# Performance work log

Hardware: AMD Instinct MI355X
Metric: run time of the kernel (lower is better)

The kernel has to match this reference:

```python
import jax, jax.numpy as jnp
import numpy as np

HEADS = 8
EPS = 1e-6
LN_EPS = 1e-5


def avg_pool(x, k):
    b, c, h, w = x.shape
    return x.reshape(b, c, h // k, k, w // k, k).mean(axis=(3, 5))


def layernorm(x, g, b):
    mu = x.mean(-1, keepdims=True)
    var = x.var(-1, keepdims=True)
    return (x - mu) / jnp.sqrt(var + LN_EPS) * g + b


def pos_embed_2d(h, w, c):
    # original calls build_2d_sincos_position_embedding(w=h, h=w): grid over (h, w), row-major flatten
    gw, gh = jnp.meshgrid(jnp.arange(h, dtype=jnp.float32),
                          jnp.arange(w, dtype=jnp.float32), indexing='ij')
    pd = c // 4
    omega = 1.0 / (10000.0 ** (jnp.arange(pd, dtype=jnp.float32) / pd))
    ow = gw.reshape(-1, 1) * omega  # (h*w, pd)
    oh = gh.reshape(-1, 1) * omega
    return jnp.concatenate([jnp.sin(ow), jnp.cos(ow), jnp.sin(oh), jnp.cos(oh)], axis=1)  # (h*w, c)


def _forward(a3, a4, q_w, q_b, q_ln_g, q_ln_b, k_w, k_b, k_ln_g, k_ln_b,
             v_w, v_b, out_w, out_b, lin1_w, lin1_b, lin2_w, lin2_b,
             n1_g, n1_b, n2_g, n2_b, idx):
    orig_a3 = a3
    if idx == 2:
        a3d = avg_pool(a3, 2)
    else:
        a3d = avg_pool(a3, 4)
        a4 = avg_pool(a4, 2)
    bs, c, h, w = a3d.shape
    L = h * w  # tgt_len == src_len (a3_down and a4 have equal spatial size)
    hd = c // HEADS

    residual = a3d.reshape(bs, c, L).transpose(0, 2, 1)  # (b, L, c)
    x3 = residual
    x4 = a4.reshape(bs, c, L).transpose(0, 2, 1)
    pos = pos_embed_2d(h, w, c)  # (L, c)
    x3 = x3 + pos[None]
    x4 = x4 + pos[None]

    Q = layernorm(x3 @ q_w + q_b, q_ln_g, q_ln_b)
    K = layernorm(x4 @ k_w + k_b, k_ln_g, k_ln_b)
    V = x4 @ v_w + v_b
    Q = jax.nn.relu(Q).reshape(bs, L, HEADS, hd).transpose(0, 2, 1, 3)  # (b,h,L,d)
    K = jax.nn.relu(K).reshape(bs, L, HEADS, hd).transpose(0, 2, 1, 3)
    V = V.reshape(bs, L, HEADS, hd).transpose(0, 2, 1, 3)

    # cosFormer position reweighting: index = pi/2 * (1..m) / m
    m = L
    wi = (np.pi / 2.0) * jnp.arange(1, m + 1, dtype=jnp.float32) / m  # (m,)
    sn = jnp.sin(wi)[None, None, :, None]
    cs = jnp.cos(wi)[None, None, :, None]
    Q_ = jnp.concatenate([Q * sn, Q * cs], axis=-1)  # (b,h,L,2d)
    K_ = jnp.concatenate([K * sn, K * cs], axis=-1)

    KV = jnp.einsum('bhld,bhlm->bhdm', K_, V)                     # (b,h,2d,d)
    Z = 1.0 / jnp.maximum(jnp.einsum('bhld,bhd->bhl', Q_, K_.sum(axis=2)), EPS)
    attn = jnp.einsum('bhld,bhdm->bhlm', Q_, KV) * Z[..., None]   # (b,h,L,d)
    attn = attn.transpose(0, 2, 1, 3).reshape(bs, L, c)

    out = attn @ out_w + out_b
    out = layernorm(out, n1_g, n1_b)     # normalize_before=False -> norm1 applied
    out = residual + out                 # dropout=0
    res2 = out
    out = jax.nn.gelu(out @ lin1_w + lin1_b, approximate=False) @ lin2_w + lin2_b
    out = layernorm(out, n2_g, n2_b)
    out = res2 + out

    a3sa = out.transpose(0, 2, 1).reshape(bs, c, h, w)
    a3sa = jax.image.resize(a3sa, orig_a3.shape, method='bilinear')  # align_corners=False
    return a3sa * orig_a3


def setup_inputs() -> dict:
    key = jax.random.key(0)
    ks = jax.random.split(key, 10)
    B, C = 16, 256
    C4 = 4 * C

    def w(k, shp):
        return jax.random.normal(k, shp, dtype=jnp.float32) * 0.02

    return {
        'a3': jax.random.normal(ks[0], (B, C, 128, 128), dtype=jnp.float32),
        'a4': jax.random.normal(ks[1], (B, C, 64, 64), dtype=jnp.float32),
        'q_w': w(ks[2], (C, C)), 'q_b': jnp.zeros((C,), jnp.float32),
        'q_ln_g': jnp.ones((C,), jnp.float32), 'q_ln_b': jnp.zeros((C,), jnp.float32),
        'k_w': w(ks[3], (C, C)), 'k_b': jnp.zeros((C,), jnp.float32),
        'k_ln_g': jnp.ones((C,), jnp.float32), 'k_ln_b': jnp.zeros((C,), jnp.float32),
        'v_w': w(ks[4], (C, C)), 'v_b': jnp.zeros((C,), jnp.float32),
        'out_w': w(ks[5], (C, C)), 'out_b': jnp.zeros((C,), jnp.float32),
        'lin1_w': w(ks[6], (C, C4)), 'lin1_b': jnp.zeros((C4,), jnp.float32),
        'lin2_w': w(ks[7], (C4, C)), 'lin2_b': jnp.zeros((C,), jnp.float32),
        'n1_g': jnp.ones((C,), jnp.float32), 'n1_b': jnp.zeros((C,), jnp.float32),
        'n2_g': jnp.ones((C,), jnp.float32), 'n2_b': jnp.zeros((C,), jnp.float32),
        'idx': 2,
    }


def reference(a3, a4, q_w, q_b, q_ln_g, q_ln_b, k_w, k_b, k_ln_g, k_ln_b,
              v_w, v_b, out_w, out_b, lin1_w, lin1_b, lin2_w, lin2_b,
              n1_g, n1_b, n2_g, n2_b, idx):
    return _forward(a3, a4, q_w, q_b, q_ln_g, q_ln_b, k_w, k_b, k_ln_g, k_ln_b,
                    v_w, v_b, out_w, out_b, lin1_w, lin1_b, lin2_w, lin2_b,
                    n1_g, n1_b, n2_g, n2_b, idx)
```

## Files before the change

kernel.cpp:

```cpp
#include <hip/hip_runtime.h>
#include <hip/hip_bf16.h>
#include <math.h>

#define HEADS 8
#define LL 4096
#define CDIM 256
#define BATCH 16
#define NROWS (BATCH*LL)

typedef __attribute__((ext_vector_type(8))) __bf16 bf16x8;
typedef __attribute__((ext_vector_type(4))) float f32x4;

__device__ inline float b2f(ushort u) {
    union { unsigned u; float f; } v; v.u = ((unsigned)u) << 16; return v.f;
}
__device__ inline ushort f2b(float f) {
    union { float f; unsigned u; } v; v.f = f;
    unsigned r = (v.u + 0x7FFF + ((v.u >> 16) & 1)) >> 16;
    return (ushort)r;
}
__device__ inline void gload16(const void* g, void* l) {
    __builtin_amdgcn_global_load_lds(
        (const __attribute__((address_space(1))) unsigned int*)g,
        (__attribute__((address_space(3))) unsigned int*)l, 16, 0, 0);
}
template<int N> __device__ inline void wait_vmcnt() {
    asm volatile("s_waitcnt vmcnt(%0)" :: "n"(N) : "memory");
}
__device__ inline float fast_gelu(float v) {
    float u = 0.7978845608028654f * v * (1.0f + 0.044715f * v * v);
    float e = exp2f(u * 2.885390081777927f);
    float t = 1.0f - 2.0f / (e + 1.0f);
    return 0.5f * v * (1.0f + t);
}

__global__ __launch_bounds__(256) void prep_kernel(
    float* __restrict__ pos, float* __restrict__ snc,
    const float* __restrict__ q_w, const float* __restrict__ k_w,
    const float* __restrict__ v_w, const float* __restrict__ o_w,
    const float* __restrict__ w1, const float* __restrict__ w2,
    ushort* __restrict__ wqT, ushort* __restrict__ wkT,
    ushort* __restrict__ wvT, ushort* __restrict__ woT,
    ushort* __restrict__ w1T, ushort* __restrict__ w2T,
    float* __restrict__ ksglob)
{
    __shared__ float t[32][33];
    int bid = blockIdx.x;
    int tid = threadIdx.x;
    if (bid == 1792) {
        for (int i = tid; i < BATCH * 2 * 256; i += 256) ksglob[i] = 0.0f;
        return;
    }
    if (bid < 1024) {
        int c = tid;
        int k = c & 63;
        float omega = expf(-(float)k * (9.210340371976184f / 64.0f));
        #pragma unroll
        for (int i = 0; i < 4; ++i) {
            int l = bid * 4 + i;
            int y = l >> 6, x = l & 63;
            float coord = (c < 128) ? (float)y : (float)x;
            float ang = coord * omega;
            float val = ((c & 127) < 64) ? sinf(ang) : cosf(ang);
            pos[l * CDIM + c] = val;
            if (c < 2) {
                float wi = 1.5707963267948966f * (float)(l + 1) / (float)LL;
                snc[l * 2 + c] = (c == 0) ? sinf(wi) : cosf(wi);
            }
        }
        return;
    }
    int id = bid - 1024;
    const float* W; ushort* Wt; int K, N, kb, nb;
    if (id < 64)       { W = q_w; Wt = wqT; K = 256;  N = 256;  kb = (id & 7) * 32;  nb = (id >> 3) * 32; }
    else if (id < 128) { id -= 64;  W = k_w; Wt = wkT; K = 256;  N = 256;  kb = (id & 7) * 32;  nb = (id >> 3) * 32; }
    else if (id < 192) { id -= 128; W = v_w; Wt = wvT; K = 256;  N = 256;  kb = (id & 7) * 32;  nb = (id >> 3) * 32; }
    else if (id < 256) { id -= 192; W = o_w; Wt = woT; K = 256;  N = 256;  kb = (id & 7) * 32;  nb = (id >> 3) * 32; }
    else if (id < 512) { id -= 256; W = w1;  Wt = w1T; K = 256;  N = 1024; kb = (id & 7) * 32;  nb = (id >> 3) * 32; }
    else               { id -= 512; W = w2;  Wt = w2T; K = 1024; N = 256;  kb = (id & 31) * 32; nb = (id >> 5) * 32; }
    int x = tid & 31, y = tid >> 5;
    #pragma unroll
    for (int i = 0; i < 4; ++i)
        t[y + i * 8][x] = W[(size_t)(kb + y + i * 8) * N + nb + x];
    __syncthreads();
    #pragma unroll
    for (int i = 0; i < 4; ++i) {
        int n = y + i * 8;
        Wt[(size_t)(nb + n) * K + kb + x] = f2b(t[x][n]);
    }
}

__global__ __launch_bounds__(256) void pool_x3_kernel(
    const float* __restrict__ a3, ushort* __restrict__ residual,
    ushort* __restrict__ x3b, const float* __restrict__ pos)
{
    __shared__ float raw[64][128];
    __shared__ float pooled[64][65];
    int i = blockIdx.x, ct = blockIdx.y, b = blockIdx.z;
    int tid = threadIdx.x;
    #pragma unroll
    for (int it = 0; it < 8; ++it) {
        int lin = (it * 256 + tid) * 4;
        int x = lin & 127;
        int cc = lin >> 7;
        size_t base = ((size_t)(b * 256 + ct * 64 + cc) * 128 + 2 * i) * 128 + x;
        float4 v0 = *(const float4*)&a3[base];
        float4 v1 = *(const float4*)&a3[base + 128];
        float4 s = make_float4(v0.x + v1.x, v0.y + v1.y, v0.z + v1.z, v0.w + v1.w);
        *(float4*)&raw[cc][x] = s;
    }
    __syncthreads();
    #pragma unroll
    for (int it = 0; it < 16; ++it) {
        int idx = it * 256 + tid;
        int j = idx & 63, cc = idx >> 6;
        pooled[cc][j] = 0.25f * (raw[cc][2 * j] + raw[cc][2 * j + 1]);
    }
    __syncthreads();
    #pragma unroll
    for (int it = 0; it < 16; ++it) {
        int cc = tid & 63;
        int jj = (tid >> 6) + it * 4;
        float val = pooled[cc][jj];
        int l = i * 64 + jj;
        int c = ct * 64 + cc;
        size_t o = (size_t)(b * LL + l) * CDIM + c;
        residual[o] = f2b(val);
        x3b[o] = f2b(val + pos[l * CDIM + c]);
    }
}

__global__ __launch_bounds__(256) void x4_kernel(
    const float* __restrict__ a4, ushort* __restrict__ x4b, const float* __restrict__ pos)
{
    __shared__ float t2[64][65];
    int y = blockIdx.x, ct = blockIdx.y, b = blockIdx.z, tid = threadIdx.x;
    #pragma unroll
    for (int it = 0; it < 16; ++it) {
        int idx = it * 256 + tid;
        int x = idx & 63, cc = idx >> 6;
        t2[cc][x] = a4[((size_t)(b * 256 + ct * 64 + cc) * 64 + y) * 64 + x];
    }
    __syncthreads();
    #pragma unroll
    for (int it = 0; it < 16; ++it) {
        int cc = tid & 63;
        int xx = (tid >> 6) + it * 4;
        int l = y * 64 + xx, c = ct * 64 + cc;
        x4b[(size_t)(b * LL + l) * CDIM + c] = f2b(t2[cc][xx] + pos[l * CDIM + c]);
    }
}

template<int KSTEPS, bool DO_LN, bool DO_RELU, bool DO_GELU, bool DO_RES, bool DO_KSUM>
__global__ __launch_bounds__(512, 2) void gemm_mfma(
    const ushort* __restrict__ A, const ushort* __restrict__ Wt,
    const float* __restrict__ bias, const float* __restrict__ gam_,
    const float* __restrict__ bet_, const ushort* __restrict__ res,
    const float* __restrict__ snc, float* __restrict__ ksglob,
    ushort* __restrict__ outb, int colsTot)
{
    constexpr int K = KSTEPS * 32;
    __shared__ ushort As[3][128 * 32];
    __shared__ ushort Bs[3][256 * 32];
    __shared__ float redS[128][4];
    __shared__ float redQ[128][4];
    __shared__ float2 mustd[128];

    const int tid = threadIdx.x;
    const int lane = tid & 63;
    const int wv = tid >> 6;
    const int wr = wv >> 2;
    const int wc = wv & 3;
    const int wvu = __builtin_amdgcn_readfirstlane(wv);
    const int row0 = blockIdx.x * 128;
    const int cbBase = blockIdx.y * 256;

    const int sr = tid >> 2;
    const int sg = (tid & 3) ^ ((sr >> 1) & 3);
    const ushort* aSrc = A + (size_t)(row0 + sr) * K + sg * 8;
    const ushort* bSrc0 = Wt + (size_t)(cbBase + sr) * K + sg * 8;
    const ushort* bSrc1 = Wt + (size_t)(cbBase + 128 + sr) * K + sg * 8;

    const int frSlot = (lane >> 4) ^ (((lane & 15) >> 1) & 3);

    auto issue = [&](int t, int buf) {
        gload16(aSrc + t * 32, (char*)&As[buf][0] + wvu * 1024);
        gload16(bSrc0 + t * 32, (char*)&Bs[buf][0] + wvu * 1024);
        gload16(bSrc1 + t * 32, (char*)&Bs[buf][0] + 8192 + wvu * 1024);
    };

    f32x4 acc[4][4] = {};
    issue(0, 0); issue(1, 1);
    #pragma unroll
    for (int t = 0; t < KSTEPS; ++t) {
        if (t < KSTEPS - 1) wait_vmcnt<3>(); else wait_vmcnt<0>();
        __builtin_amdgcn_s_barrier();
        if (t + 2 < KSTEPS) issue(t + 2, (t + 2) % 3);
        const int cb = t % 3;
        bf16x8 af[4], bfr[4];
        #pragma unroll
        for (int f = 0; f < 4; ++f) {
            int r = wr * 64 + f * 16 + (lane & 15);
            af[f] = *(const bf16x8*)&As[cb][r * 32 + frSlot * 8];
            int c = wc * 64 + f * 16 + (lane & 15);
            bfr[f] = *(const bf16x8*)&Bs[cb][c * 32 + frSlot * 8];
        }
        #pragma unroll
        for (int fi = 0; fi < 4; ++fi)
            #pragma unroll
            for (int fj = 0; fj < 4; ++fj)
                acc[fi][fj] = __builtin_amdgcn_mfma_f32_16x16x32_bf16(
                    af[fi], bfr[fj], acc[fi][fj], 0, 0, 0);
    }
    __syncthreads();

    const int cl = lane & 15;
    const int rg = lane >> 4;
    float bia[4], gmv[4], btv[4];
    #pragma unroll
    for (int fj = 0; fj < 4; ++fj) {
        int col = cbBase + wc * 64 + fj * 16 + cl;
        bia[fj] = bias[col];
        if constexpr (DO_LN) { gmv[fj] = gam_[col]; btv[fj] = bet_[col]; }
    }
    #pragma unroll
    for (int fi = 0; fi < 4; ++fi)
        #pragma unroll
        for (int fj = 0; fj < 4; ++fj)
            #pragma unroll
            for (int j = 0; j < 4; ++j)
                acc[fi][fj][j] += bia[fj];

    if constexpr (DO_LN) {
        #pragma unroll
        for (int fi = 0; fi < 4; ++fi)
            #pragma unroll
            for (int j = 0; j < 4; ++j) {
                float s = acc[fi][0][j] + acc[fi][1][j] + acc[fi][2][j] + acc[fi][3][j];
                float q = acc[fi][0][j] * acc[fi][0][j] + acc[fi][1][j] * acc[fi][1][j]
                        + acc[fi][2][j] * acc[fi][2][j] + acc[fi][3][j] * acc[fi][3][j];
                #pragma unroll
                for (int m = 1; m <= 8; m <<= 1) {
                    s += __shfl_xor(s, m, 64);
                    q += __shfl_xor(q, m, 64);
                }
                if (cl == 0) {
                    int tr = wr * 64 + fi * 16 + rg * 4 + j;
                    redS[tr][wc] = s; redQ[tr][wc] = q;
                }
            }
        __syncthreads();
        if (tid < 128) {
            float s = redS[tid][0] + redS[tid][1] + redS[tid][2] + redS[tid][3];
            float q = redQ[tid][0] + redQ[tid][1] + redQ[tid][2] + redQ[tid][3];
            float mu = s * (1.0f / 256.0f);
            float var = q * (1.0f / 256.0f) - mu * mu;
            mustd[tid] = make_float2(mu, rsqrtf(var + 1e-5f));
        }
        __syncthreads();
        #pragma unroll
        for (int fi = 0; fi < 4; ++fi)
            #pragma unroll
            for (int j = 0; j < 4; ++j) {
                float2 ms = mustd[wr * 64 + fi * 16 + rg * 4 + j];
                #pragma unroll
                for (int fj = 0; fj < 4; ++fj)
                    acc[fi][fj][j] = (acc[fi][fj][j] - ms.x) * ms.y * gmv[fj] + btv[fj];
            }
    }
    if constexpr (DO_RELU) {
        #pragma unroll
        for (int fi = 0; fi < 4; ++fi)
            #pragma unroll
            for (int fj = 0; fj < 4; ++fj)
                #pragma unroll
                for (int j = 0; j < 4; ++j)
                    acc[fi][fj][j] = fmaxf(acc[fi][fj][j], 0.0f);
    }
    if constexpr (DO_GELU) {
        #pragma unroll
        for (int fi = 0; fi < 4; ++fi)
            #pragma unroll
            for (int fj = 0; fj < 4; ++fj)
                #pragma unroll
                for (int j = 0; j < 4; ++j)
                    acc[fi][fj][j] = fast_gelu(acc[fi][fj][j]);
    }
    float kss[4] = {}, ksc[4] = {};
    #pragma unroll
    for (int fi = 0; fi < 4; ++fi)
        #pragma unroll
        for (int j = 0; j < 4; ++j) {
            int rloc = wr * 64 + fi * 16 + rg * 4 + j;
            size_t row = row0 + rloc;
            size_t rbase = row * (size_t)colsTot + cbBase + wc * 64 + cl;
            float sn, cs;
            if constexpr (DO_KSUM) {
                int l = (int)(row & (LL - 1));
                sn = snc[l * 2]; cs = snc[l * 2 + 1];
            }
            #pragma unroll
            for (int fj = 0; fj < 4; ++fj) {
                float v = acc[fi][fj][j];
                if constexpr (DO_RES) v += b2f(res[rbase + fj * 16]);
                outb[rbase + fj * 16] = f2b(v);
                if constexpr (DO_KSUM) { kss[fj] += sn * v; ksc[fj] += cs * v; }
            }
        }
    if constexpr (DO_KSUM) {
        int b = row0 >> 12;
        #pragma unroll
        for (int fj = 0; fj < 4; ++fj) {
            float s = kss[fj], c = ksc[fj];
            s += __shfl_xor(s, 16, 64); s += __shfl_xor(s, 32, 64);
            c += __shfl_xor(c, 16, 64); c += __shfl_xor(c, 32, 64);
            if (rg == 0) {
                int col = wc * 64 + fj * 16 + cl;
                atomicAdd(&ksglob[((size_t)b * 2 + 0) * 256 + col], s);
                atomicAdd(&ksglob[((size_t)b * 2 + 1) * 256 + col], c);
            }
        }
    }
}

__global__ __launch_bounds__(256) void kv_kernel(
    const ushort* __restrict__ Kmat, const ushort* __restrict__ Vmat,
    const float* __restrict__ snc, float* __restrict__ kvpart)
{
    __shared__ float Kt[64][36];
    __shared__ float Vt[64][36];
    __shared__ float sns[64], css[64];
    int chunk = blockIdx.x;
    int bh = blockIdx.y;
    int b = bh >> 3, h = bh & 7;
    int tid = threadIdx.x;
    int m = tid & 31;
    int d0 = (tid >> 5) * 4;
    float accs[4] = {}, accc[4] = {};
    int l0chunk = chunk * 512;
    int lrow = tid >> 2;
    int lcol = (tid & 3) * 8;
    for (int sub = 0; sub < 8; ++sub) {
        int l0 = l0chunk + sub * 64;
        {
            size_t gbase = (size_t)(b * LL + l0 + lrow) * CDIM + h * 32 + lcol;
            uint4 kr = *(const uint4*)&Kmat[gbase];
            uint4 vr = *(const uint4*)&Vmat[gbase];
            float* kd = &Kt[lrow][lcol];
            float* vd = &Vt[lrow][lcol];
            kd[0] = b2f((ushort)(kr.x & 0xffff)); kd[1] = b2f((ushort)(kr.x >> 16));
            kd[2] = b2f((ushort)(kr.y & 0xffff)); kd[3] = b2f((ushort)(kr.y >> 16));
            kd[4] = b2f((ushort)(kr.z & 0xffff)); kd[5] = b2f((ushort)(kr.z >> 16));
            kd[6] = b2f((ushort)(kr.w & 0xffff)); kd[7] = b2f((ushort)(kr.w >> 16));
            vd[0] = b2f((ushort)(vr.x & 0xffff)); vd[1] = b2f((ushort)(vr.x >> 16));
            vd[2] = b2f((ushort)(vr.y & 0xffff)); vd[3] = b2f((ushort)(vr.y >> 16));
            vd[4] = b2f((ushort)(vr.z & 0xffff)); vd[5] = b2f((ushort)(vr.z >> 16));
            vd[6] = b2f((ushort)(vr.w & 0xffff)); vd[7] = b2f((ushort)(vr.w >> 16));
        }
        if (tid < 64) { sns[tid] = snc[(l0 + tid) * 2]; css[tid] = snc[(l0 + tid) * 2 + 1]; }
        __syncthreads();
        #pragma unroll 4
        for (int lt = 0; lt < 64; ++lt) {
            float v = Vt[lt][m];
            float vs = v * sns[lt];
            float vc = v * css[lt];
            float4 kd4 = *(const float4*)&Kt[lt][d0];
            accs[0] += kd4.x * vs; accc[0] += kd4.x * vc;
            accs[1] += kd4.y * vs; accc[1] += kd4.y * vc;
            accs[2] += kd4.z * vs; accc[2] += kd4.z * vc;
            accs[3] += kd4.w * vs; accc[3] += kd4.w * vc;
        }
        __syncthreads();
    }
    size_t base = (size_t)(bh * 8 + chunk) * 2048;
    #pragma unroll
    for (int i2 = 0; i2 < 4; ++i2) {
        kvpart[base + (d0 + i2) * 32 + m] = accs[i2];
        kvpart[base + 1024 + (d0 + i2) * 32 + m] = accc[i2];
    }
}

__global__ __launch_bounds__(256) void kvred_kernel(
    const float* __restrict__ kvpart, const float* __restrict__ ksglob,
    ushort* __restrict__ Bimg)
{
    int bh = blockIdx.x;
    int b = bh >> 3, h = bh & 7;
    int tid = threadIdx.x;
    for (int e = tid; e < 2560; e += 256) {
        int n = e >> 5;
        int k = e & 31;
        int t = n >> 4, col = n & 15;
        float v = 0.0f;
        if (t < 4) {
            int off = (t >= 2 ? 1024 : 0) + k * 32 + (t & 1) * 16 + col;
            #pragma unroll
            for (int ch = 0; ch < 8; ++ch)
                v += kvpart[(size_t)(bh * 8 + ch) * 2048 + off];
        } else if (col < 2) {
            v = ksglob[((size_t)b * 2 + col) * 256 + h * 32 + k];
        }
        ushort hi = f2b(v);
        ushort lo = f2b(v - b2f(hi));
        Bimg[(size_t)bh * 5120 + n * 32 + k] = hi;
        Bimg[(size_t)bh * 5120 + (80 + n) * 32 + k] = lo;
    }
}

__global__ __launch_bounds__(256, 2) void attn_mfma(
    const ushort* __restrict__ Qmat, const ushort* __restrict__ Bimg,
    const float* __restrict__ snc, ushort* __restrict__ attnOut)
{
    __shared__ ushort Bs[5120];
    int ltile = blockIdx.x, h = blockIdx.y, b = blockIdx.z;
    int bh = b * 8 + h;
    int tid = threadIdx.x;
    int lane = tid & 63;
    int wv = tid >> 6;

    for (int e = tid; e < 640; e += 256)
        *(uint4*)&Bs[e * 8] = *(const uint4*)&Bimg[(size_t)bh * 5120 + e * 8];
    __syncthreads();

    bf16x8 bfr[10];
    #pragma unroll
    for (int tt = 0; tt < 10; ++tt) {
        int row = (tt < 5 ? tt * 16 : 80 + (tt - 5) * 16) + (lane & 15);
        bfr[tt] = *(const bf16x8*)&Bs[row * 32 + (lane >> 4) * 8];
    }
    int lbase = ltile * 256 + wv * 64;
    bf16x8 af[4];
    #pragma unroll
    for (int fi = 0; fi < 4; ++fi) {
        int l = lbase + fi * 16 + (lane & 15);
        af[fi] = *(const bf16x8*)&Qmat[(size_t)(b * LL + l) * CDIM + h * 32 + (lane >> 4) * 8];
    }
    f32x4 acc[4][5] = {};
    #pragma unroll
    for (int fi = 0; fi < 4; ++fi)
        #pragma unroll
        for (int t = 0; t < 5; ++t) {
            acc[fi][t] = __builtin_amdgcn_mfma_f32_16x16x32_bf16(af[fi], bfr[t], acc[fi][t], 0, 0, 0);
            acc[fi][t] = __builtin_amdgcn_mfma_f32_16x16x32_bf16(af[fi], bfr[t + 5], acc[fi][t], 0, 0, 0);
        }

    int zlane = lane & 48;
    int cl = lane & 15;
    #pragma unroll
    for (int fi = 0; fi < 4; ++fi) {
        #pragma unroll
        for (int j = 0; j < 4; ++j) {
            float zraw = acc[fi][4][j];
            float zs = __shfl(zraw, zlane, 64);
            float zc = __shfl(zraw, zlane | 1, 64);
            int l = lbase + fi * 16 + ((lane >> 4) & 3) * 4 + j;
            float sn = snc[l * 2], cs = snc[l * 2 + 1];
            float den = sn * zs + cs * zc;
            float Z = 1.0f / fmaxf(den, 1e-6f);
            float v0 = (sn * acc[fi][0][j] + cs * acc[fi][2][j]) * Z;
            float v1 = (sn * acc[fi][1][j] + cs * acc[fi][3][j]) * Z;
            size_t ob = (size_t)(b * LL + l) * CDIM + h * 32 + cl;
            attnOut[ob] = f2b(v0);
            attnOut[ob + 16] = f2b(v1);
        }
    }
}

__global__ __launch_bounds__(256) void resize_mul_kernel(
    const ushort* __restrict__ ffeat, const float* __restrict__ a3, float* __restrict__ out)
{
    __shared__ float ft[3][64][65];
    int k = blockIdx.x, ct = blockIdx.y, b = blockIdx.z;
    int tid = threadIdx.x;
    for (int it = 0; it < 48; ++it) {
        int e = it * 256 + tid;
        int cc = e & 63;
        int xs = (e >> 6) & 63;
        int ys = e >> 12;
        int ysrc = min(max(k - 1 + ys, 0), 63);
        ft[ys][cc][xs] = b2f(ffeat[(size_t)(b * LL + ysrc * 64 + xs) * CDIM + ct * 64 + cc]);
    }
    __syncthreads();
    int x = tid & 127;
    int half = tid >> 7;
    int y = 2 * k + half;
    int ysA, ysB; float wyA, wyB;
    if (half == 0) { ysA = 0; ysB = 1; wyA = 0.25f; wyB = 0.75f; }
    else           { ysA = 1; ysB = 2; wyA = 0.75f; wyB = 0.25f; }
    int x0; float wx1;
    if ((x & 1) == 0) { x0 = x / 2 - 1; wx1 = 0.75f; }
    else              { x0 = x / 2;     wx1 = 0.25f; }
    int x0c = max(x0, 0);
    int x1c = min(x0 + 1, 63);
    float wx0 = 1.0f - wx1;
    for (int cc = 0; cc < 64; ++cc) {
        float rA = wx0 * ft[ysA][cc][x0c] + wx1 * ft[ysA][cc][x1c];
        float rB = wx0 * ft[ysB][cc][x0c] + wx1 * ft[ysB][cc][x1c];
        float val = wyA * rA + wyB * rB;
        size_t oidx = ((size_t)(b * 256 + ct * 64 + cc) * 128 + y) * 128 + x;
        out[oidx] = val * a3[oidx];
    }
}

extern "C" void kernel_launch(void* const* d_in, const int* in_sizes, int n_in,
                              void* d_out, int out_size, void* d_ws, size_t ws_size,
                              hipStream_t stream)
{
    const float* a3     = (const float*)d_in[0];
    const float* a4     = (const float*)d_in[1];
    const float* q_w    = (const float*)d_in[2];
    const float* q_b    = (const float*)d_in[3];
    const float* q_ln_g = (const float*)d_in[4];
    const float* q_ln_b = (const float*)d_in[5];
    const float* k_w    = (const float*)d_in[6];
    const float* k_b    = (const float*)d_in[7];
    const float* k_ln_g = (const float*)d_in[8];
    const float* k_ln_b = (const float*)d_in[9];
    const float* v_w    = (const float*)d_in[10];
    const float* v_b    = (const float*)d_in[11];
    const float* out_w  = (const float*)d_in[12];
    const float* out_b  = (const float*)d_in[13];
    const float* lin1_w = (const float*)d_in[14];
    const float* lin1_b = (const float*)d_in[15];
    const float* lin2_w = (const float*)d_in[16];
    const float* lin2_b = (const float*)d_in[17];
    const float* n1_g   = (const float*)d_in[18];
    const float* n1_b   = (const float*)d_in[19];
    const float* n2_g   = (const float*)d_in[20];
    const float* n2_b   = (const float*)d_in[21];
    float* out = (float*)d_out;
    char* base = (char*)d_ws;

    const size_t MiB = 1024 * 1024;
    float*  pos      = (float*)(base);
    float*  snc      = (float*)(base + 4 * MiB);
    ushort* wqT      = (ushort*)(base + 4 * MiB + 64 * 1024);
    ushort* wkT      = wqT + 256 * 256;
    ushort* wvT      = wkT + 256 * 256;
    ushort* woT      = wvT + 256 * 256;
    ushort* w1T      = woT + 256 * 256;
    ushort* w2T      = w1T + 1024 * 256;
    ushort* residual = (ushort*)(base + 6 * MiB);
    ushort* x3b      = (ushort*)(base + 38 * MiB);
    ushort* x4b      = (ushort*)(base + 70 * MiB);
    ushort* Qb       = (ushort*)(base + 102 * MiB);
    ushort* Kb       = (ushort*)(base + 134 * MiB);
    ushort* Vb       = (ushort*)(base + 166 * MiB);
    float*  kvp      = (float*)(base + 198 * MiB);
    float*  ksglob   = (float*)(base + 206 * MiB);
    ushort* Bimg     = (ushort*)(base + 207 * MiB);
    ushort* h1b      = (ushort*)(base + 209 * MiB);
    ushort* attnb    = x3b;
    ushort* res2b    = x4b;
    ushort* ffeat    = residual;

    prep_kernel<<<1793, 256, 0, stream>>>(pos, snc, q_w, k_w, v_w, out_w, lin1_w, lin2_w,
                                          wqT, wkT, wvT, woT, w1T, w2T, ksglob);
    pool_x3_kernel<<<dim3(64, 4, 16), 256, 0, stream>>>(a3, residual, x3b, pos);
    x4_kernel<<<dim3(64, 4, 16), 256, 0, stream>>>(a4, x4b, pos);

    gemm_mfma<8, true, true, false, false, false><<<dim3(NROWS / 128, 1), 512, 0, stream>>>(
        x3b, wqT, q_b, q_ln_g, q_ln_b, nullptr, nullptr, nullptr, Qb, 256);
    gemm_mfma<8, true, true, false, false, true><<<dim3(NROWS / 128, 1), 512, 0, stream>>>(
        x4b, wkT, k_b, k_ln_g, k_ln_b, nullptr, snc, ksglob, Kb, 256);
    gemm_mfma<8, false, false, false, false, false><<<dim3(NROWS / 128, 1), 512, 0, stream>>>(
        x4b, wvT, v_b, nullptr, nullptr, nullptr, nullptr, nullptr, Vb, 256);

    kv_kernel<<<dim3(8, 128), 256, 0, stream>>>(Kb, Vb, snc, kvp);
    kvred_kernel<<<128, 256, 0, stream>>>(kvp, ksglob, Bimg);
    attn_mfma<<<dim3(16, 8, 16), 256, 0, stream>>>(Qb, Bimg, snc, attnb);

    gemm_mfma<8, true, false, false, true, false><<<dim3(NROWS / 128, 1), 512, 0, stream>>>(
        attnb, woT, out_b, n1_g, n1_b, residual, nullptr, nullptr, res2b, 256);
    gemm_mfma<8, false, false, true, false, false><<<dim3(NROWS / 128, 4), 512, 0, stream>>>(
        res2b, w1T, lin1_b, nullptr, nullptr, nullptr, nullptr, nullptr, h1b, 1024);
    gemm_mfma<32, true, false, false, true, false><<<dim3(NROWS / 128, 1), 512, 0, stream>>>(
        h1b, w2T, lin2_b, n2_g, n2_b, res2b, nullptr, nullptr, ffeat, 256);

    resize_mul_kernel<<<dim3(64, 4, 16), 256, 0, stream>>>(ffeat, a3, out);
}
```

Before: 587.3 us.

## Stage whole weight blocks in LDS, stream A from registers, fuse pooling kernels

The GEMM now loads a full 256x256 bf16 weight block (pre-swizzled by the prep kernel) into LDS once per K-chunk. The A operand is read directly from global memory into registers with double buffering, replacing the triple-buffered async A/B tile pipeline. The x3 pooling and x4 transpose kernels are merged into one launch, MFMA sections get s_setprio hints, and the resize kernel reads bf16 features with vectorized 16-byte loads. The 128 KiB LDS footprint limits occupancy per CU, and unstaged A loads rely on cache for reuse across waves.

```diff
diff --git a/kernel.cpp b/kernel.cpp
--- a/kernel.cpp
+++ b/kernel.cpp
@@ -23,9 +23,6 @@
     __builtin_amdgcn_global_load_lds(
         (const __attribute__((address_space(1))) unsigned int*)g,
         (__attribute__((address_space(3))) unsigned int*)l, 16, 0, 0);
-}
-template<int N> __device__ inline void wait_vmcnt() {
-    asm volatile("s_waitcnt vmcnt(%0)" :: "n"(N) : "memory");
 }
 __device__ inline float fast_gelu(float v) {
     float u = 0.7978845608028654f * v * (1.0f + 0.044715f * v * v);
@@ -71,13 +68,13 @@
         return;
     }
     int id = bid - 1024;
-    const float* W; ushort* Wt; int K, N, kb, nb;
-    if (id < 64)       { W = q_w; Wt = wqT; K = 256;  N = 256;  kb = (id & 7) * 32;  nb = (id >> 3) * 32; }
-    else if (id < 128) { id -= 64;  W = k_w; Wt = wkT; K = 256;  N = 256;  kb = (id & 7) * 32;  nb = (id >> 3) * 32; }
-    else if (id < 192) { id -= 128; W = v_w; Wt = wvT; K = 256;  N = 256;  kb = (id & 7) * 32;  nb = (id >> 3) * 32; }
-    else if (id < 256) { id -= 192; W = o_w; Wt = woT; K = 256;  N = 256;  kb = (id & 7) * 32;  nb = (id >> 3) * 32; }
-    else if (id < 512) { id -= 256; W = w1;  Wt = w1T; K = 256;  N = 1024; kb = (id & 7) * 32;  nb = (id >> 3) * 32; }
-    else               { id -= 512; W = w2;  Wt = w2T; K = 1024; N = 256;  kb = (id & 31) * 32; nb = (id >> 5) * 32; }
+    const float* W; ushort* Wt; int K, N, kb, nb, mode;
+    if (id < 64)       { W = q_w; Wt = wqT; K = 256;  N = 256;  kb = (id & 7) * 32;  nb = (id >> 3) * 32; mode = 0; }
+    else if (id < 128) { id -= 64;  W = k_w; Wt = wkT; K = 256;  N = 256;  kb = (id & 7) * 32;  nb = (id >> 3) * 32; mode = 0; }
+    else if (id < 192) { id -= 128; W = v_w; Wt = wvT; K = 256;  N = 256;  kb = (id & 7) * 32;  nb = (id >> 3) * 32; mode = 0; }
+    else if (id < 256) { id -= 192; W = o_w; Wt = woT; K = 256;  N = 256;  kb = (id & 7) * 32;  nb = (id >> 3) * 32; mode = 0; }
+    else if (id < 512) { id -= 256; W = w1;  Wt = w1T; K = 256;  N = 1024; kb = (id & 7) * 32;  nb = (id >> 3) * 32; mode = 1; }
+    else               { id -= 512; W = w2;  Wt = w2T; K = 1024; N = 256;  kb = (id & 31) * 32; nb = (id >> 5) * 32; mode = 2; }
     int x = tid & 31, y = tid >> 5;
     #pragma unroll
     for (int i = 0; i < 4; ++i)
@@ -86,82 +83,86 @@
     #pragma unroll
     for (int i = 0; i < 4; ++i) {
         int n = y + i * 8;
-        Wt[(size_t)(nb + n) * K + kb + x] = f2b(t[x][n]);
-    }
-}
-
-__global__ __launch_bounds__(256) void pool_x3_kernel(
-    const float* __restrict__ a3, ushort* __restrict__ residual,
-    ushort* __restrict__ x3b, const float* __restrict__ pos)
+        int k = kb + x, col = nb + n;
+        int Wb, colIn, kin;
+        if (mode == 1)      { Wb = col >> 8; colIn = col & 255; kin = k; }
+        else if (mode == 2) { Wb = k >> 8;   colIn = col;       kin = k & 255; }
+        else                { Wb = 0;        colIn = col;       kin = k; }
+        size_t idx = (size_t)Wb * 65536 + colIn * 256
+                   + ((((kin >> 3) ^ (colIn & 7)) << 3) | (kin & 7));
+        Wt[idx] = f2b(t[x][n]);
+    }
+}
+
+__global__ __launch_bounds__(256) void pool_x4_kernel(
+    const float* __restrict__ a3, const float* __restrict__ a4,
+    ushort* __restrict__ residual, ushort* __restrict__ x3b,
+    ushort* __restrict__ x4b, const float* __restrict__ pos)
 {
     __shared__ float raw[64][128];
     __shared__ float pooled[64][65];
-    int i = blockIdx.x, ct = blockIdx.y, b = blockIdx.z;
     int tid = threadIdx.x;
-    #pragma unroll
-    for (int it = 0; it < 8; ++it) {
-        int lin = (it * 256 + tid) * 4;
-        int x = lin & 127;
-        int cc = lin >> 7;
-        size_t base = ((size_t)(b * 256 + ct * 64 + cc) * 128 + 2 * i) * 128 + x;
-        float4 v0 = *(const float4*)&a3[base];
-        float4 v1 = *(const float4*)&a3[base + 128];
-        float4 s = make_float4(v0.x + v1.x, v0.y + v1.y, v0.z + v1.z, v0.w + v1.w);
-        *(float4*)&raw[cc][x] = s;
-    }
-    __syncthreads();
-    #pragma unroll
-    for (int it = 0; it < 16; ++it) {
-        int idx = it * 256 + tid;
-        int j = idx & 63, cc = idx >> 6;
-        pooled[cc][j] = 0.25f * (raw[cc][2 * j] + raw[cc][2 * j + 1]);
-    }
-    __syncthreads();
-    #pragma unroll
-    for (int it = 0; it < 16; ++it) {
-        int cc = tid & 63;
-        int jj = (tid >> 6) + it * 4;
-        float val = pooled[cc][jj];
-        int l = i * 64 + jj;
-        int c = ct * 64 + cc;
-        size_t o = (size_t)(b * LL + l) * CDIM + c;
-        residual[o] = f2b(val);
-        x3b[o] = f2b(val + pos[l * CDIM + c]);
-    }
-}
-
-__global__ __launch_bounds__(256) void x4_kernel(
-    const float* __restrict__ a4, ushort* __restrict__ x4b, const float* __restrict__ pos)
-{
-    __shared__ float t2[64][65];
-    int y = blockIdx.x, ct = blockIdx.y, b = blockIdx.z, tid = threadIdx.x;
-    #pragma unroll
-    for (int it = 0; it < 16; ++it) {
-        int idx = it * 256 + tid;
-        int x = idx & 63, cc = idx >> 6;
-        t2[cc][x] = a4[((size_t)(b * 256 + ct * 64 + cc) * 64 + y) * 64 + x];
-    }
-    __syncthreads();
-    #pragma unroll
-    for (int it = 0; it < 16; ++it) {
-        int cc = tid & 63;
-        int xx = (tid >> 6) + it * 4;
-        int l = y * 64 + xx, c = ct * 64 + cc;
-        x4b[(size_t)(b * LL + l) * CDIM + c] = f2b(t2[cc][xx] + pos[l * CDIM + c]);
-    }
-}
-
-template<int KSTEPS, bool DO_LN, bool DO_RELU, bool DO_GELU, bool DO_RES, bool DO_KSUM>
-__global__ __launch_bounds__(512, 2) void gemm_mfma(
-    const ushort* __restrict__ A, const ushort* __restrict__ Wt,
+    int ct = blockIdx.y;
+    if (blockIdx.z < 16) {
+        int i = blockIdx.x, b = blockIdx.z;
+        #pragma unroll
+        for (int it = 0; it < 8; ++it) {
+            int lin = (it * 256 + tid) * 4;
+            int x = lin & 127;
+            int cc = lin >> 7;
+            size_t base = ((size_t)(b * 256 + ct * 64 + cc) * 128 + 2 * i) * 128 + x;
+            float4 v0 = *(const float4*)&a3[base];
+            float4 v1 = *(const float4*)&a3[base + 128];
+            float4 s = make_float4(v0.x + v1.x, v0.y + v1.y, v0.z + v1.z, v0.w + v1.w);
+            *(float4*)&raw[cc][x] = s;
+        }
+        __syncthreads();
+        #pragma unroll
+        for (int it = 0; it < 16; ++it) {
+            int idx = it * 256 + tid;
+            int j = idx & 63, cc = idx >> 6;
+            pooled[cc][j] = 0.25f * (raw[cc][2 * j] + raw[cc][2 * j + 1]);
+        }
+        __syncthreads();
+        #pragma unroll
+        for (int it = 0; it < 16; ++it) {
+            int cc = tid & 63;
+            int jj = (tid >> 6) + it * 4;
+            float val = pooled[cc][jj];
+            int l = i * 64 + jj;
+            int c = ct * 64 + cc;
+            size_t o = (size_t)(b * LL + l) * CDIM + c;
+            residual[o] = f2b(val);
+            x3b[o] = f2b(val + pos[l * CDIM + c]);
+        }
+    } else {
+        int y = blockIdx.x, b = blockIdx.z - 16;
+        #pragma unroll
+        for (int it = 0; it < 16; ++it) {
+            int idx = it * 256 + tid;
+            int x = idx & 63, cc = idx >> 6;
+            pooled[cc][x] = a4[((size_t)(b * 256 + ct * 64 + cc) * 64 + y) * 64 + x];
+        }
+        __syncthreads();
+        #pragma unroll
+        for (int it = 0; it < 16; ++it) {
+            int cc = tid & 63;
+            int xx = (tid >> 6) + it * 4;
+            int l = y * 64 + xx, c = ct * 64 + cc;
+            x4b[(size_t)(b * LL + l) * CDIM + c] = f2b(pooled[cc][xx] + pos[l * CDIM + c]);
+        }
+    }
+}
+
+template<int KCH, bool DO_LN, bool DO_RELU, bool DO_GELU, bool DO_RES, bool DO_KSUM>
+__global__ __launch_bounds__(512, 2) void gemm_wlds(
+    const ushort* __restrict__ A, const ushort* __restrict__ Wblk,
     const float* __restrict__ bias, const float* __restrict__ gam_,
     const float* __restrict__ bet_, const ushort* __restrict__ res,
     const float* __restrict__ snc, float* __restrict__ ksglob,
-    ushort* __restrict__ outb, int colsTot)
-{
-    constexpr int K = KSTEPS * 32;
-    __shared__ ushort As[3][128 * 32];
-    __shared__ ushort Bs[3][256 * 32];
+    ushort* __restrict__ outb, int colsTot, int aStride)
+{
+    __shared__ ushort Ws[256 * 256];
     __shared__ float redS[128][4];
     __shared__ float redQ[128][4];
     __shared__ float2 mustd[128];
@@ -174,48 +175,67 @@
     const int wvu = __builtin_amdgcn_readfirstlane(wv);
     const int row0 = blockIdx.x * 128;
     const int cbBase = blockIdx.y * 256;
-
-    const int sr = tid >> 2;
-    const int sg = (tid & 3) ^ ((sr >> 1) & 3);
-    const ushort* aSrc = A + (size_t)(row0 + sr) * K + sg * 8;
-    const ushort* bSrc0 = Wt + (size_t)(cbBase + sr) * K + sg * 8;
-    const ushort* bSrc1 = Wt + (size_t)(cbBase + 128 + sr) * K + sg * 8;
-
-    const int frSlot = (lane >> 4) ^ (((lane & 15) >> 1) & 3);
-
-    auto issue = [&](int t, int buf) {
-        gload16(aSrc + t * 32, (char*)&As[buf][0] + wvu * 1024);
-        gload16(bSrc0 + t * 32, (char*)&Bs[buf][0] + wvu * 1024);
-        gload16(bSrc1 + t * 32, (char*)&Bs[buf][0] + 8192 + wvu * 1024);
+    const int r15 = lane & 15;
+    const int kg = lane >> 4;
+
+    const ushort* rp[4];
+    #pragma unroll
+    for (int fi = 0; fi < 4; ++fi)
+        rp[fi] = A + (size_t)(row0 + wr * 64 + fi * 16 + r15) * aStride + kg * 8;
+
+    f32x4 acc[4][4] = {};
+
+    auto loadA = [&](bf16x8 (&dst)[4], int off) {
+        #pragma unroll
+        for (int fi = 0; fi < 4; ++fi)
+            dst[fi] = *(const bf16x8*)(rp[fi] + off);
     };
-
-    f32x4 acc[4][4] = {};
-    issue(0, 0); issue(1, 1);
-    #pragma unroll
-    for (int t = 0; t < KSTEPS; ++t) {
-        if (t < KSTEPS - 1) wait_vmcnt<3>(); else wait_vmcnt<0>();
-        __builtin_amdgcn_s_barrier();
-        if (t + 2 < KSTEPS) issue(t + 2, (t + 2) % 3);
-        const int cb = t % 3;
-        bf16x8 af[4], bfr[4];
+    auto dostep = [&](int t, bf16x8 (&aCur)[4]) {
+        bf16x8 bfr[4];
         #pragma unroll
         for (int f = 0; f < 4; ++f) {
-            int r = wr * 64 + f * 16 + (lane & 15);
-            af[f] = *(const bf16x8*)&As[cb][r * 32 + frSlot * 8];
-            int c = wc * 64 + f * 16 + (lane & 15);
-            bfr[f] = *(const bf16x8*)&Bs[cb][c * 32 + frSlot * 8];
-        }
+            int c = wc * 64 + f * 16 + r15;
+            int slot = (t * 4 + kg) ^ (c & 7);
+            bfr[f] = *(const bf16x8*)&Ws[c * 256 + slot * 8];
+        }
+        __builtin_amdgcn_s_setprio(1);
         #pragma unroll
         for (int fi = 0; fi < 4; ++fi)
             #pragma unroll
             for (int fj = 0; fj < 4; ++fj)
                 acc[fi][fj] = __builtin_amdgcn_mfma_f32_16x16x32_bf16(
-                    af[fi], bfr[fj], acc[fi][fj], 0, 0, 0);
+                    aCur[fi], bfr[fj], acc[fi][fj], 0, 0, 0);
+        __builtin_amdgcn_s_setprio(0);
+    };
+
+    #pragma unroll
+    for (int ch = 0; ch < KCH; ++ch) {
+        if (ch > 0) __syncthreads();
+        {
+            const ushort* wsg = Wblk + (size_t)(blockIdx.y * KCH + ch) * 65536;
+            #pragma unroll
+            for (int s = 0; s < 16; ++s)
+                gload16(wsg + s * 4096 + tid * 8,
+                        (char*)&Ws[0] + s * 8192 + wvu * 1024);
+        }
+        __syncthreads();
+
+        const int chOff = ch * 256;
+        bf16x8 aA[4], aB[4];
+        loadA(aA, chOff);
+        loadA(aB, chOff + 32);
+        #pragma unroll
+        for (int tp = 0; tp < 4; ++tp) {
+            dostep(2 * tp, aA);
+            if (2 * tp + 2 < 8) loadA(aA, chOff + (2 * tp + 2) * 32);
+            dostep(2 * tp + 1, aB);
+            if (2 * tp + 3 < 8) loadA(aB, chOff + (2 * tp + 3) * 32);
+        }
     }
     __syncthreads();
 
-    const int cl = lane & 15;
-    const int rg = lane >> 4;
+    const int cl = r15;
+    const int rg = kg;
     float bia[4], gmv[4], btv[4];
     #pragma unroll
     for (int fj = 0; fj < 4; ++fj) {
@@ -436,6 +456,7 @@
         af[fi] = *(const bf16x8*)&Qmat[(size_t)(b * LL + l) * CDIM + h * 32 + (lane >> 4) * 8];
     }
     f32x4 acc[4][5] = {};
+    __builtin_amdgcn_s_setprio(1);
     #pragma unroll
     for (int fi = 0; fi < 4; ++fi)
         #pragma unroll
@@ -443,6 +464,7 @@
             acc[fi][t] = __builtin_amdgcn_mfma_f32_16x16x32_bf16(af[fi], bfr[t], acc[fi][t], 0, 0, 0);
             acc[fi][t] = __builtin_amdgcn_mfma_f32_16x16x32_bf16(af[fi], bfr[t + 5], acc[fi][t], 0, 0, 0);
         }
+    __builtin_amdgcn_s_setprio(0);
 
     int zlane = lane & 48;
     int cl = lane & 15;
@@ -472,13 +494,19 @@
     __shared__ float ft[3][64][65];
     int k = blockIdx.x, ct = blockIdx.y, b = blockIdx.z;
     int tid = threadIdx.x;
-    for (int it = 0; it < 48; ++it) {
+    #pragma unroll
+    for (int it = 0; it < 6; ++it) {
         int e = it * 256 + tid;
-        int cc = e & 63;
-        int xs = (e >> 6) & 63;
-        int ys = e >> 12;
+        int cg = e & 7;
+        int xs = (e >> 3) & 63;
+        int ys = e >> 9;
         int ysrc = min(max(k - 1 + ys, 0), 63);
-        ft[ys][cc][xs] = b2f(ffeat[(size_t)(b * LL + ysrc * 64 + xs) * CDIM + ct * 64 + cc]);
+        uint4 raw = *(const uint4*)&ffeat[(size_t)(b * LL + ysrc * 64 + xs) * CDIM + ct * 64 + cg * 8];
+        float* dst = &ft[ys][cg * 8][xs];
+        dst[0]   = b2f((ushort)(raw.x & 0xffff)); dst[65]  = b2f((ushort)(raw.x >> 16));
+        dst[130] = b2f((ushort)(raw.y & 0xffff)); dst[195] = b2f((ushort)(raw.y >> 16));
+        dst[260] = b2f((ushort)(raw.z & 0xffff)); dst[325] = b2f((ushort)(raw.z >> 16));
+        dst[390] = b2f((ushort)(raw.w & 0xffff)); dst[455] = b2f((ushort)(raw.w >> 16));
     }
     __syncthreads();
     int x = tid & 127;
@@ -556,26 +584,25 @@
 
     prep_kernel<<<1793, 256, 0, stream>>>(pos, snc, q_w, k_w, v_w, out_w, lin1_w, lin2_w,
                                           wqT, wkT, wvT, woT, w1T, w2T, ksglob);
-    pool_x3_kernel<<<dim3(64, 4, 16), 256, 0, stream>>>(a3, residual, x3b, pos);
-    x4_kernel<<<dim3(64, 4, 16), 256, 0, stream>>>(a4, x4b, pos);
-
-    gemm_mfma<8, true, true, false, false, false><<<dim3(NROWS / 128, 1), 512, 0, stream>>>(
-        x3b, wqT, q_b, q_ln_g, q_ln_b, nullptr, nullptr, nullptr, Qb, 256);
-    gemm_mfma<8, true, true, false, false, true><<<dim3(NROWS / 128, 1), 512, 0, stream>>>(
-        x4b, wkT, k_b, k_ln_g, k_ln_b, nullptr, snc, ksglob, Kb, 256);
-    gemm_mfma<8, false, false, false, false, false><<<dim3(NROWS / 128, 1), 512, 0, stream>>>(
-        x4b, wvT, v_b, nullptr, nullptr, nullptr, nullptr, nullptr, Vb, 256);
+    pool_x4_kernel<<<dim3(64, 4, 32), 256, 0, stream>>>(a3, a4, residual, x3b, x4b, pos);
+
+    gemm_wlds<1, true, true, false, false, false><<<dim3(NROWS / 128, 1), 512, 0, stream>>>(
+        x3b, wqT, q_b, q_ln_g, q_ln_b, nullptr, nullptr, nullptr, Qb, 256, 256);
+    gemm_wlds<1, true, true, false, false, true><<<dim3(NROWS / 128, 1), 512, 0, stream>>>(
+        x4b, wkT, k_b, k_ln_g, k_ln_b, nullptr, snc, ksglob, Kb, 256, 256);
+    gemm_wlds<1, false, false, false, false, false><<<dim3(NROWS / 128, 1), 512, 0, stream>>>(
+        x4b, wvT, v_b, nullptr, nullptr, nullptr, nullptr, nullptr, Vb, 256, 256);
 
     kv_kernel<<<dim3(8, 128), 256, 0, stream>>>(Kb, Vb, snc, kvp);
     kvred_kernel<<<128, 256, 0, stream>>>(kvp, ksglob, Bimg);
     attn_mfma<<<dim3(16, 8, 16), 256, 0, stream>>>(Qb, Bimg, snc, attnb);
 
-    gemm_mfma<8, true, false, false, true, false><<<dim3(NROWS / 128, 1), 512, 0, stream>>>(
-        attnb, woT, out_b, n1_g, n1_b, residual, nullptr, nullptr, res2b, 256);
-    gemm_mfma<8, false, false, true, false, false><<<dim3(NROWS / 128, 4), 512, 0, stream>>>(
-        res2b, w1T, lin1_b, nullptr, nullptr, nullptr, nullptr, nullptr, h1b, 1024);
-    gemm_mfma<32, true, false, false, true, false><<<dim3(NROWS / 128, 1), 512, 0, stream>>>(
-        h1b, w2T, lin2_b, n2_g, n2_b, res2b, nullptr, nullptr, ffeat, 256);
+    gemm_wlds<1, true, false, false, true, false><<<dim3(NROWS / 128, 1), 512, 0, stream>>>(
+        attnb, woT, out_b, n1_g, n1_b, residual, nullptr, nullptr, res2b, 256, 256);
+    gemm_wlds<1, false, false, true, false, false><<<dim3(NROWS / 128, 4), 512, 0, stream>>>(
+        res2b, w1T, lin1_b, nullptr, nullptr, nullptr, nullptr, nullptr, h1b, 1024, 256);
+    gemm_wlds<4, true, false, false, true, false><<<dim3(NROWS / 128, 1), 512, 0, stream>>>(
+        h1b, w2T, lin2_b, n2_g, n2_b, res2b, nullptr, nullptr, ffeat, 256, 1024);
 
     resize_mul_kernel<<<dim3(64, 4, 16), 256, 0, stream>>>(ffeat, a3, out);
 }
```

Result: slower. 652.5 us (+11.1%).
